# Performance work log

Hardware: AMD Instinct MI355X
Metric: run time of the kernel (lower is better)

## Reference

```python
import jax, jax.numpy as jnp
from jax import lax
import numpy as np

T, B, H, I = 128, 128, 1024, 2048  # seq, batch, hidden, lstm input (=2*H)


def lstm(x, w_ih, w_hh, b_ih, b_hh):
    """PyTorch-semantics single-layer LSTM, zero init state.
    x: [T,B,I]; w_ih: [4H,I]; w_hh: [4H,H]; gate order i,f,g,o."""
    Th, Bh = x.shape[0], x.shape[1]
    Hh = w_hh.shape[1]
    # input projection for all timesteps at once (the big GEMM)
    xp = jnp.einsum('tbi,gi->tbg', x, w_ih) + b_ih + b_hh  # [T,B,4H]

    def step(carry, xt):
        h, c = carry
        gates = xt + h @ w_hh.T  # [B,4H]
        i, f, g, o = jnp.split(gates, 4, axis=-1)
        i = jax.nn.sigmoid(i)
        f = jax.nn.sigmoid(f)
        g = jnp.tanh(g)
        o = jax.nn.sigmoid(o)
        c = f * c + i * g
        h = o * jnp.tanh(c)
        return (h, c), h

    h0 = jnp.zeros((Bh, Hh), x.dtype)
    (_, _), hs = lax.scan(step, (h0, h0), xp)
    return hs  # [T,B,H]


def setup_inputs() -> dict:
    key = jax.random.key(0)
    ks = jax.random.split(key, 10)
    s = 0.03  # ~ uniform(-1/sqrt(H), 1/sqrt(H)) scale of torch LSTM init
    return {
        'input4': jax.random.normal(ks[0], (T, B, H), jnp.float32),
        'input0': jax.random.normal(ks[1], (T, B, H), jnp.float32),
        'w_ih6': jax.random.normal(ks[2], (4 * H, I), jnp.float32) * s,
        'w_hh6': jax.random.normal(ks[3], (4 * H, H), jnp.float32) * s,
        'b_ih6': jax.random.normal(ks[4], (4 * H,), jnp.float32) * s,
        'b_hh6': jax.random.normal(ks[5], (4 * H,), jnp.float32) * s,
        'w_ih10': jax.random.normal(ks[6], (4 * H, I), jnp.float32) * s,
        'w_hh10': jax.random.normal(ks[7], (4 * H, H), jnp.float32) * s,
        'b_ih10': jax.random.normal(ks[8], (4 * H,), jnp.float32) * s,
        'b_hh10': jax.random.normal(ks[9], (4 * H,), jnp.float32) * s,
    }


def reference(input4, input0, w_ih6, w_hh6, b_ih6, b_hh6, w_ih10, w_hh10, b_ih10, b_hh10):
    out1 = input4
    out5 = jnp.concatenate([input0, out1], axis=2)        # [T,B,2H]
    out7 = lstm(out5, w_ih6, w_hh6, b_ih6, b_hh6)          # [T,B,H]
    out8 = out7  # dropout p=0.2 -> identity in eval/inference
    out9 = jnp.concatenate([out8, out1], axis=2)           # [T,B,2H]
    out11 = lstm(out9, w_ih10, w_hh10, b_ih10, b_hh10) + out7
    out13 = out11  # dropout identity
    out14 = jnp.concatenate([out13, out1], axis=2)         # [T,B,2H]
    return (out1, out11, out14)
```

## Files before the change

kernel.cpp:

```cpp
#include <hip/hip_runtime.h>
#include <hip/hip_bf16.h>
#include <hip/hip_cooperative_groups.h>
#include <stdint.h>

namespace cg = cooperative_groups;

typedef __hip_bfloat16 bf16;
typedef __attribute__((ext_vector_type(8))) short s16x8;
typedef __attribute__((ext_vector_type(4))) float f32x4;

#define MFMA_BF16 __builtin_amdgcn_mfma_f32_16x16x32_bf16


__device__ __forceinline__ float sigmoidf_(float x) {
  return 1.0f / (1.0f + __expf(-x));
}
__device__ __forceinline__ float tanhf_(float x) {
  return 2.0f / (1.0f + __expf(-2.0f * x)) - 1.0f;
}

__device__ __forceinline__ s16x8 cvt8(const float* __restrict__ p) {
  s16x8 r;
#pragma unroll
  for (int i = 0; i < 8; i++) {
    bf16 h = __float2bfloat16(p[i]);
    r[i] = *(const short*)&h;
  }
  return r;
}

__global__ __launch_bounds__(256)
void cvt_k(const float* __restrict__ src, bf16* __restrict__ dst) {
  const size_t i = (size_t)(blockIdx.x * 256 + threadIdx.x) * 8;
  *(s16x8*)(dst + i) = cvt8(src + i);
}

__global__ __launch_bounds__(256)
void gemm_xp(const void* __restrict__ A0, int a0_bf,
             const void* __restrict__ A1, int a1_bf,
             const void* __restrict__ W, int w_bf,
             const float* __restrict__ b0, const float* __restrict__ b1,
             float* __restrict__ X, int row_base)
{
  __shared__ short As[128][32];
  __shared__ short Bs[128][32];
  const int tid = threadIdx.x;
  const int wave = tid >> 6, lane = tid & 63;
  const int lr = lane & 15, lq = lane >> 4;
  const int wm = wave >> 1, wn = wave & 1;
  const int lrow0 = blockIdx.y * 128;
  const int grow0 = row_base + lrow0;
  const int col0 = blockIdx.x * 128;

  f32x4 acc[4][4];
  const f32x4 z = {0.f, 0.f, 0.f, 0.f};
  for (int i = 0; i < 4; i++)
    for (int j = 0; j < 4; j++) acc[i][j] = z;

  const int sr = tid >> 2;
  const int skk = (tid & 3) * 8;

  for (int k0 = 0; k0 < 2048; k0 += 32) {
    if (k0 < 1024) {
      if (a0_bf) {
        const bf16* Ab = (const bf16*)A0;
        *(s16x8*)&As[sr][skk]      = *(const s16x8*)(Ab + (size_t)(grow0 + sr) * 1024 + k0 + skk);
        *(s16x8*)&As[sr + 64][skk] = *(const s16x8*)(Ab + (size_t)(grow0 + sr + 64) * 1024 + k0 + skk);
      } else {
        const float* Af = (const float*)A0;
        *(s16x8*)&As[sr][skk]      = cvt8(Af + (size_t)(grow0 + sr) * 1024 + k0 + skk);
        *(s16x8*)&As[sr + 64][skk] = cvt8(Af + (size_t)(grow0 + sr + 64) * 1024 + k0 + skk);
      }
    } else {
      const int ac = k0 - 1024;
      if (a1_bf) {
        const bf16* Ab = (const bf16*)A1;
        *(s16x8*)&As[sr][skk]      = *(const s16x8*)(Ab + (size_t)(grow0 + sr) * 1024 + ac + skk);
        *(s16x8*)&As[sr + 64][skk] = *(const s16x8*)(Ab + (size_t)(grow0 + sr + 64) * 1024 + ac + skk);
      } else {
        const float* Af = (const float*)A1;
        *(s16x8*)&As[sr][skk]      = cvt8(Af + (size_t)(grow0 + sr) * 1024 + ac + skk);
        *(s16x8*)&As[sr + 64][skk] = cvt8(Af + (size_t)(grow0 + sr + 64) * 1024 + ac + skk);
      }
    }
    if (w_bf) {
      const bf16* Wb = (const bf16*)W;
      *(s16x8*)&Bs[sr][skk]      = *(const s16x8*)(Wb + (size_t)(col0 + sr) * 2048 + k0 + skk);
      *(s16x8*)&Bs[sr + 64][skk] = *(const s16x8*)(Wb + (size_t)(col0 + sr + 64) * 2048 + k0 + skk);
    } else {
      const float* Wf = (const float*)W;
      *(s16x8*)&Bs[sr][skk]      = cvt8(Wf + (size_t)(col0 + sr) * 2048 + k0 + skk);
      *(s16x8*)&Bs[sr + 64][skk] = cvt8(Wf + (size_t)(col0 + sr + 64) * 2048 + k0 + skk);
    }
    __syncthreads();
    s16x8 bfrag[4];
    for (int nt = 0; nt < 4; nt++)
      bfrag[nt] = *(const s16x8*)&Bs[wn * 64 + nt * 16 + lr][lq * 8];
    for (int mt = 0; mt < 4; mt++) {
      s16x8 a = *(const s16x8*)&As[wm * 64 + mt * 16 + lr][lq * 8];
      for (int nt = 0; nt < 4; nt++)
        acc[mt][nt] = MFMA_BF16(a, bfrag[nt], acc[mt][nt], 0, 0, 0);
    }
    __syncthreads();
  }

  for (int mt = 0; mt < 4; mt++) {
    const int mbase = lrow0 + wm * 64 + mt * 16 + lq * 4;
    for (int nt = 0; nt < 4; nt++) {
      const int n = col0 + wn * 64 + nt * 16 + lr;
      const float bias = b0[n] + b1[n];
      for (int r = 0; r < 4; r++)
        X[(size_t)(mbase + r) * 4096 + n] = acc[mt][nt][r] + bias;
    }
  }
}

__global__ __launch_bounds__(256, 1)
void lstm_chunk(const bf16* __restrict__ w_hh,
                const float* __restrict__ xp,
                float* __restrict__ c_g,
                bf16* __restrict__ hist,
                bf16* __restrict__ h2a, bf16* __restrict__ h2b,
                const bf16* __restrict__ zero,
                const bf16* __restrict__ add_base,
                float* __restrict__ o11, float* __restrict__ o14,
                int t0, int nsteps, int layer2)
{
  __shared__ __align__(16) char WS[131072];
  const int tid = threadIdx.x;
  const int wave = tid >> 6, lane = tid & 63;
  const int lr = lane & 15, lq = lane >> 4;
  const int jb = blockIdx.x & 63, mb = blockIdx.x >> 6;
  const int j0 = jb * 16;
  const int rowb = mb * 64 + wave * 16;

  for (int i = tid; i < 8192; i += 256) {
    const int rr = i >> 7, ck = i & 127;
    const int g = rr >> 4, col = rr & 15;
    const s16x8 v = *(const s16x8*)(w_hh + ((size_t)(g * 1024 + j0 + col) << 10) + (ck << 3));
    *(s16x8*)(WS + (((rr << 11) + (ck << 4)) ^ ((rr & 7) << 4))) = v;
  }

  const int j = j0 + lr;
  const int b0r = rowb + lq * 4;
  float creg[4];
#pragma unroll
  for (int r = 0; r < 4; r++) creg[r] = c_g[(b0r + r) * 1024 + j];

  const int sw = (lr & 7) << 4;
  const int rb0 = lr << 11;
  const int rb1 = (16 + lr) << 11;
  const int rb2 = (32 + lr) << 11;
  const int rb3 = (48 + lr) << 11;

  cg::grid_group grid = cg::this_grid();
  __syncthreads();

  for (int tt = 0; tt < nsteps; ++tt) {
    const int t = t0 + tt;
    const bf16* hp;
    bf16* hn;
    if (layer2) {
      hp = (t == 0) ? zero : ((t & 1) ? h2a : h2b);
      hn = (t & 1) ? h2b : h2a;
    } else {
      hp = (t == 0) ? zero : (hist + ((size_t)(t - 1) << 17));
      hn = hist + ((size_t)t << 17);
    }

    f32x4 acc[4];
    const f32x4 z = {0.f, 0.f, 0.f, 0.f};
    acc[0] = z; acc[1] = z; acc[2] = z; acc[3] = z;

    const bf16* ap = hp + ((size_t)(rowb + lr) << 10) + lq * 8;
#pragma unroll 8
    for (int k0 = 0; k0 < 1024; k0 += 32) {
      const s16x8 a = *(const s16x8*)(ap + k0);
      const int co = (((k0 >> 3) + lq) << 4) ^ sw;
      acc[0] = MFMA_BF16(a, *(const s16x8*)(WS + rb0 + co), acc[0], 0, 0, 0);
      acc[1] = MFMA_BF16(a, *(const s16x8*)(WS + rb1 + co), acc[1], 0, 0, 0);
      acc[2] = MFMA_BF16(a, *(const s16x8*)(WS + rb2 + co), acc[2], 0, 0, 0);
      acc[3] = MFMA_BF16(a, *(const s16x8*)(WS + rb3 + co), acc[3], 0, 0, 0);
    }

    const float* xpt = xp + ((size_t)tt << 19);
#pragma unroll
    for (int r = 0; r < 4; r++) {
      const int b = b0r + r;
      const float gi = acc[0][r] + xpt[b * 4096 + j];
      const float gf = acc[1][r] + xpt[b * 4096 + 1024 + j];
      const float gg = acc[2][r] + xpt[b * 4096 + 2048 + j];
      const float go = acc[3][r] + xpt[b * 4096 + 3072 + j];
      const float i_ = sigmoidf_(gi);
      const float f_ = sigmoidf_(gf);
      const float g_ = tanhf_(gg);
      const float o_ = sigmoidf_(go);
      const float cn = f_ * creg[r] + i_ * g_;
      creg[r] = cn;
      const float hv = o_ * tanhf_(cn);
      const int idx = b * 1024 + j;
      hn[idx] = __float2bfloat16(hv);
      if (layer2) {
        const float ov = hv + __bfloat162float(add_base[((size_t)t << 17) + idx]);
        o11[((size_t)t << 17) + idx] = ov;
        o14[((size_t)t << 18) + b * 2048 + j] = ov;
      }
    }

    if (tt + 1 < nsteps) grid.sync();
  }

#pragma unroll
  for (int r = 0; r < 4; r++) c_g[(b0r + r) * 1024 + j] = creg[r];
}

__global__ __launch_bounds__(256)
void finalize_k(const float4* __restrict__ in4, float4* __restrict__ out1,
                float* __restrict__ out14)
{
  const int ci = blockIdx.x * 256 + threadIdx.x;
  float4 v = in4[ci];
  out1[ci] = v;
  const int flat = ci * 4;
  const int row = flat >> 10, j = flat & 1023;
  *(float4*)&out14[(size_t)row * 2048 + 1024 + j] = v;
}

extern "C" void kernel_launch(void* const* d_in, const int* in_sizes, int n_in,
                              void* d_out, int out_size, void* d_ws, size_t ws_size,
                              hipStream_t stream)
{
  const float* input4 = (const float*)d_in[0];
  const float* input0 = (const float*)d_in[1];
  const float* w_ih6  = (const float*)d_in[2];
  const float* w_hh6  = (const float*)d_in[3];
  const float* b_ih6  = (const float*)d_in[4];
  const float* b_hh6  = (const float*)d_in[5];
  const float* w_ih10 = (const float*)d_in[6];
  const float* w_hh10 = (const float*)d_in[7];
  const float* b_ih10 = (const float*)d_in[8];
  const float* b_hh10 = (const float*)d_in[9];

  char* ws = (char*)d_ws;
  bf16* WHH6b  = (bf16*)(ws);
  bf16* WHH10b = (bf16*)(ws + 8388608ull);
  bf16* OUT7b  = (bf16*)(ws + 16777216ull);
  bf16* ZERO   = (bf16*)(ws + 50331648ull);
  bf16* H2A    = (bf16*)(ws + 50593792ull);
  bf16* H2B    = (bf16*)(ws + 50855936ull);
  float* C1    = (float*)(ws + 51118080ull);
  float* C2    = (float*)(ws + 51642368ull);

  const size_t small_bytes = 52166656ull;
  size_t avail = (ws_size > small_bytes) ? (ws_size - small_bytes) : 0;
  const size_t bf_bytes = 83886080ull;
  int TC = 16, use_bf = 0;
  if (avail >= bf_bytes + 2097152ull) {
    use_bf = 1;
    const size_t a2 = avail - bf_bytes;
    while (TC > 1 && (size_t)TC * 2097152ull > a2) TC >>= 1;
  } else {
    while (TC > 1 && (size_t)TC * 2097152ull > avail) TC >>= 1;
  }
  const int NCH = 128 / TC;
  float* Xc  = (float*)(ws + small_bytes);
  bf16* IN0b = (bf16*)(ws + small_bytes + (size_t)TC * 2097152ull);
  bf16* IN4b = IN0b + 16777216ull;
  bf16* WIHb = IN4b + 16777216ull;

  hipMemsetAsync(ZERO, 0, 262144, stream);
  hipMemsetAsync(C1, 0, 524288, stream);
  hipMemsetAsync(C2, 0, 524288, stream);

  cvt_k<<<2048, 256, 0, stream>>>(w_hh6, WHH6b);
  cvt_k<<<2048, 256, 0, stream>>>(w_hh10, WHH10b);

  float* o1  = (float*)d_out;
  float* o11 = o1 + 16777216;
  float* o14 = o1 + 33554432;

  const dim3 ggrid(32, TC);

  if (use_bf) {
    cvt_k<<<8192, 256, 0, stream>>>(input0, IN0b);
    cvt_k<<<8192, 256, 0, stream>>>(input4, IN4b);
    cvt_k<<<4096, 256, 0, stream>>>(w_ih6, WIHb);
  }
  for (int ch = 0; ch < NCH; ++ch) {
    gemm_xp<<<ggrid, 256, 0, stream>>>(
        use_bf ? (const void*)IN0b : (const void*)input0, use_bf,
        use_bf ? (const void*)IN4b : (const void*)input4, use_bf,
        use_bf ? (const void*)WIHb : (const void*)w_ih6, use_bf,
        b_ih6, b_hh6, Xc, ch * TC * 128);
    {
      const bf16* p_whh = WHH6b; const float* p_xp = Xc; float* p_c = C1;
      bf16* p_hist = OUT7b; bf16* p_h2a = nullptr; bf16* p_h2b = nullptr;
      const bf16* p_zero = ZERO; const bf16* p_add = nullptr;
      float* p_o11 = nullptr; float* p_o14 = nullptr;
      int p_t0 = ch * TC, p_ns = TC, p_l2 = 0;
      void* args[] = {&p_whh, &p_xp, &p_c, &p_hist, &p_h2a, &p_h2b,
                      &p_zero, &p_add, &p_o11, &p_o14, &p_t0, &p_ns, &p_l2};
      hipLaunchCooperativeKernel((void*)lstm_chunk, dim3(128), dim3(256),
                                 args, 0, stream);
    }
  }

  if (use_bf) {
    cvt_k<<<4096, 256, 0, stream>>>(w_ih10, WIHb);
  }
  for (int ch = 0; ch < NCH; ++ch) {
    gemm_xp<<<ggrid, 256, 0, stream>>>(
        (const void*)OUT7b, 1,
        use_bf ? (const void*)IN4b : (const void*)input4, use_bf,
        use_bf ? (const void*)WIHb : (const void*)w_ih10, use_bf,
        b_ih10, b_hh10, Xc, ch * TC * 128);
    {
      const bf16* p_whh = WHH10b; const float* p_xp = Xc; float* p_c = C2;
      bf16* p_hist = nullptr; bf16* p_h2a = H2A; bf16* p_h2b = H2B;
      const bf16* p_zero = ZERO; const bf16* p_add = OUT7b;
      float* p_o11 = o11; float* p_o14 = o14;
      int p_t0 = ch * TC, p_ns = TC, p_l2 = 1;
      void* args[] = {&p_whh, &p_xp, &p_c, &p_hist, &p_h2a, &p_h2b,
                      &p_zero, &p_add, &p_o11, &p_o14, &p_t0, &p_ns, &p_l2};
      hipLaunchCooperativeKernel((void*)lstm_chunk, dim3(128), dim3(256),
                                 args, 0, stream);
    }
  }

  finalize_k<<<16384, 256, 0, stream>>>((const float4*)input4, (float4*)d_out, o14);
}
```

Measured before the change: 7.402 ms.

## Replace cooperative grid.sync with custom atomic barrier and halve LSTM block size

Swaps cg::grid_sync for a hand-written global barrier. It uses a monotonically increasing counter with a release flag and sleep polling, and h stores are made with system-scope atomics so they are visible across blocks. Each block now runs 2 waves instead of 4, and every wave computes two 16-row M tiles, so each W_hh LDS fragment is reused twice. Layer 2 can write its h history into a separate full buffer instead of ping-pong buffers, and the time chunk grows from 16 to 32 steps, which means fewer launches. The aim is to cut barrier and launch overhead on the serial recurrence. The risks are relaxed-ordering correctness of the custom barrier and lower latency hiding with fewer waves per block.

Result: faster. 6.044 ms (-18.3%).

```diff
diff --git a/kernel.cpp b/kernel.cpp
--- a/kernel.cpp
+++ b/kernel.cpp
@@ -1,15 +1,13 @@
 #include <hip/hip_runtime.h>
 #include <hip/hip_bf16.h>
-#include <hip/hip_cooperative_groups.h>
 #include <stdint.h>
-
-namespace cg = cooperative_groups;
 
 typedef __hip_bfloat16 bf16;
 typedef __attribute__((ext_vector_type(8))) short s16x8;
 typedef __attribute__((ext_vector_type(4))) float f32x4;
 
 #define MFMA_BF16 __builtin_amdgcn_mfma_f32_16x16x32_bf16
+#define NB 128
 
 
 __device__ __forceinline__ float sigmoidf_(float x) {
@@ -115,7 +113,27 @@
   }
 }
 
-__global__ __launch_bounds__(256, 1)
+__device__ __forceinline__ void gbar_sync(unsigned* bar, unsigned target) {
+  asm volatile("s_waitcnt vmcnt(0)" ::: "memory");
+  __syncthreads();
+  if (threadIdx.x == 0) {
+    unsigned old = __hip_atomic_fetch_add(&bar[0], 1u, __ATOMIC_RELAXED,
+                                          __HIP_MEMORY_SCOPE_SYSTEM);
+    if (old == target - 1u) {
+      __hip_atomic_store(&bar[64], target, __ATOMIC_RELAXED,
+                         __HIP_MEMORY_SCOPE_SYSTEM);
+    } else {
+      while (__hip_atomic_load(&bar[64], __ATOMIC_RELAXED,
+                               __HIP_MEMORY_SCOPE_SYSTEM) < target) {
+        __builtin_amdgcn_s_sleep(1);
+      }
+    }
+    __builtin_amdgcn_fence(__ATOMIC_ACQUIRE, "agent");
+  }
+  __syncthreads();
+}
+
+__global__ __launch_bounds__(128, 1)
 void lstm_chunk(const bf16* __restrict__ w_hh,
                 const float* __restrict__ xp,
                 float* __restrict__ c_g,
@@ -124,6 +142,7 @@
                 const bf16* __restrict__ zero,
                 const bf16* __restrict__ add_base,
                 float* __restrict__ o11, float* __restrict__ o14,
+                unsigned* __restrict__ bar, unsigned gbase,
                 int t0, int nsteps, int layer2)
 {
   __shared__ __align__(16) char WS[131072];
@@ -132,9 +151,9 @@
   const int lr = lane & 15, lq = lane >> 4;
   const int jb = blockIdx.x & 63, mb = blockIdx.x >> 6;
   const int j0 = jb * 16;
-  const int rowb = mb * 64 + wave * 16;
-
-  for (int i = tid; i < 8192; i += 256) {
+  const int wrow = mb * 64 + wave * 32;
+
+  for (int i = tid; i < 8192; i += 128) {
     const int rr = i >> 7, ck = i & 127;
     const int g = rr >> 4, col = rr & 15;
     const s16x8 v = *(const s16x8*)(w_hh + ((size_t)(g * 1024 + j0 + col) << 10) + (ck << 3));
@@ -142,76 +161,96 @@
   }
 
   const int j = j0 + lr;
-  const int b0r = rowb + lq * 4;
-  float creg[4];
-#pragma unroll
-  for (int r = 0; r < 4; r++) creg[r] = c_g[(b0r + r) * 1024 + j];
-
   const int sw = (lr & 7) << 4;
-  const int rb0 = lr << 11;
-  const int rb1 = (16 + lr) << 11;
-  const int rb2 = (32 + lr) << 11;
-  const int rb3 = (48 + lr) << 11;
-
-  cg::grid_group grid = cg::this_grid();
+  int rbg[4];
+#pragma unroll
+  for (int g = 0; g < 4; g++) rbg[g] = (g * 16 + lr) << 11;
+
+  float creg[2][4];
+#pragma unroll
+  for (int mt = 0; mt < 2; mt++)
+#pragma unroll
+    for (int r = 0; r < 4; r++)
+      creg[mt][r] = c_g[(wrow + mt * 16 + lq * 4 + r) * 1024 + j];
+
   __syncthreads();
 
   for (int tt = 0; tt < nsteps; ++tt) {
     const int t = t0 + tt;
     const bf16* hp;
     bf16* hn;
-    if (layer2) {
+    if (hist) {
+      hp = (t == 0) ? zero : (hist + ((size_t)(t - 1) << 17));
+      hn = hist + ((size_t)t << 17);
+    } else {
       hp = (t == 0) ? zero : ((t & 1) ? h2a : h2b);
       hn = (t & 1) ? h2b : h2a;
-    } else {
-      hp = (t == 0) ? zero : (hist + ((size_t)(t - 1) << 17));
-      hn = hist + ((size_t)t << 17);
-    }
-
-    f32x4 acc[4];
+    }
+
+    f32x4 acc[2][4];
     const f32x4 z = {0.f, 0.f, 0.f, 0.f};
-    acc[0] = z; acc[1] = z; acc[2] = z; acc[3] = z;
-
-    const bf16* ap = hp + ((size_t)(rowb + lr) << 10) + lq * 8;
+#pragma unroll
+    for (int mt = 0; mt < 2; mt++)
+#pragma unroll
+      for (int g = 0; g < 4; g++) acc[mt][g] = z;
+
+    const bf16* ap0 = hp + ((size_t)(wrow + lr) << 10) + lq * 8;
 #pragma unroll 8
     for (int k0 = 0; k0 < 1024; k0 += 32) {
-      const s16x8 a = *(const s16x8*)(ap + k0);
+      const s16x8 a0 = *(const s16x8*)(ap0 + k0);
+      const s16x8 a1 = *(const s16x8*)(ap0 + 16384 + k0);
       const int co = (((k0 >> 3) + lq) << 4) ^ sw;
-      acc[0] = MFMA_BF16(a, *(const s16x8*)(WS + rb0 + co), acc[0], 0, 0, 0);
-      acc[1] = MFMA_BF16(a, *(const s16x8*)(WS + rb1 + co), acc[1], 0, 0, 0);
-      acc[2] = MFMA_BF16(a, *(const s16x8*)(WS + rb2 + co), acc[2], 0, 0, 0);
-      acc[3] = MFMA_BF16(a, *(const s16x8*)(WS + rb3 + co), acc[3], 0, 0, 0);
+      s16x8 b[4];
+#pragma unroll
+      for (int g = 0; g < 4; g++)
+        b[g] = *(const s16x8*)(WS + rbg[g] + co);
+#pragma unroll
+      for (int g = 0; g < 4; g++)
+        acc[0][g] = MFMA_BF16(a0, b[g], acc[0][g], 0, 0, 0);
+#pragma unroll
+      for (int g = 0; g < 4; g++)
+        acc[1][g] = MFMA_BF16(a1, b[g], acc[1][g], 0, 0, 0);
     }
 
     const float* xpt = xp + ((size_t)tt << 19);
 #pragma unroll
-    for (int r = 0; r < 4; r++) {
-      const int b = b0r + r;
-      const float gi = acc[0][r] + xpt[b * 4096 + j];
-      const float gf = acc[1][r] + xpt[b * 4096 + 1024 + j];
-      const float gg = acc[2][r] + xpt[b * 4096 + 2048 + j];
-      const float go = acc[3][r] + xpt[b * 4096 + 3072 + j];
-      const float i_ = sigmoidf_(gi);
-      const float f_ = sigmoidf_(gf);
-      const float g_ = tanhf_(gg);
-      const float o_ = sigmoidf_(go);
-      const float cn = f_ * creg[r] + i_ * g_;
-      creg[r] = cn;
-      const float hv = o_ * tanhf_(cn);
-      const int idx = b * 1024 + j;
-      hn[idx] = __float2bfloat16(hv);
-      if (layer2) {
-        const float ov = hv + __bfloat162float(add_base[((size_t)t << 17) + idx]);
-        o11[((size_t)t << 17) + idx] = ov;
-        o14[((size_t)t << 18) + b * 2048 + j] = ov;
+    for (int mt = 0; mt < 2; mt++) {
+#pragma unroll
+      for (int r = 0; r < 4; r++) {
+        const int b = wrow + mt * 16 + lq * 4 + r;
+        const float gi = acc[mt][0][r] + xpt[b * 4096 + j];
+        const float gf = acc[mt][1][r] + xpt[b * 4096 + 1024 + j];
+        const float gg = acc[mt][2][r] + xpt[b * 4096 + 2048 + j];
+        const float go = acc[mt][3][r] + xpt[b * 4096 + 3072 + j];
+        const float i_ = sigmoidf_(gi);
+        const float f_ = sigmoidf_(gf);
+        const float g_ = tanhf_(gg);
+        const float o_ = sigmoidf_(go);
+        const float cn = f_ * creg[mt][r] + i_ * g_;
+        creg[mt][r] = cn;
+        const float hv = o_ * tanhf_(cn);
+        const int idx = b * 1024 + j;
+        bf16 hb = __float2bfloat16(hv);
+        __hip_atomic_store((unsigned short*)(hn + idx),
+                           *(unsigned short*)&hb,
+                           __ATOMIC_RELAXED, __HIP_MEMORY_SCOPE_SYSTEM);
+        if (layer2) {
+          const float ov = hv + __bfloat162float(add_base[((size_t)t << 17) + idx]);
+          o11[((size_t)t << 17) + idx] = ov;
+          o14[((size_t)t << 18) + b * 2048 + j] = ov;
+        }
       }
     }
 
-    if (tt + 1 < nsteps) grid.sync();
-  }
-
-#pragma unroll
-  for (int r = 0; r < 4; r++) c_g[(b0r + r) * 1024 + j] = creg[r];
+    if (tt + 1 < nsteps)
+      gbar_sync(bar, gbase + (unsigned)(tt + 1) * NB);
+  }
+
+#pragma unroll
+  for (int mt = 0; mt < 2; mt++)
+#pragma unroll
+    for (int r = 0; r < 4; r++)
+      c_g[(wrow + mt * 16 + lq * 4 + r) * 1024 + j] = creg[mt][r];
 }
 
 __global__ __launch_bounds__(256)
@@ -250,11 +289,21 @@
   bf16* H2B    = (bf16*)(ws + 50855936ull);
   float* C1    = (float*)(ws + 51118080ull);
   float* C2    = (float*)(ws + 51642368ull);
-
-  const size_t small_bytes = 52166656ull;
-  size_t avail = (ws_size > small_bytes) ? (ws_size - small_bytes) : 0;
+  unsigned* BAR = (unsigned*)(ws + 52166656ull);
+
+  const size_t base_end = 52170752ull;
+  size_t avail = (ws_size > base_end) ? (ws_size - base_end) : 0;
+  size_t off = base_end;
+  int use_h2h = 0;
+  bf16* H2H = nullptr;
+  if (avail >= 33554432ull + 2097152ull) {
+    use_h2h = 1;
+    H2H = (bf16*)(ws + off);
+    off += 33554432ull;
+    avail -= 33554432ull;
+  }
   const size_t bf_bytes = 83886080ull;
-  int TC = 16, use_bf = 0;
+  int TC = 32, use_bf = 0;
   if (avail >= bf_bytes + 2097152ull) {
     use_bf = 1;
     const size_t a2 = avail - bf_bytes;
@@ -263,14 +312,15 @@
     while (TC > 1 && (size_t)TC * 2097152ull > avail) TC >>= 1;
   }
   const int NCH = 128 / TC;
-  float* Xc  = (float*)(ws + small_bytes);
-  bf16* IN0b = (bf16*)(ws + small_bytes + (size_t)TC * 2097152ull);
+  float* Xc  = (float*)(ws + off);
+  bf16* IN0b = (bf16*)(ws + off + (size_t)TC * 2097152ull);
   bf16* IN4b = IN0b + 16777216ull;
   bf16* WIHb = IN4b + 16777216ull;
 
   hipMemsetAsync(ZERO, 0, 262144, stream);
   hipMemsetAsync(C1, 0, 524288, stream);
   hipMemsetAsync(C2, 0, 524288, stream);
+  hipMemsetAsync(BAR, 0, 4096, stream);
 
   cvt_k<<<2048, 256, 0, stream>>>(w_hh6, WHH6b);
   cvt_k<<<2048, 256, 0, stream>>>(w_hh10, WHH10b);
@@ -280,6 +330,7 @@
   float* o14 = o1 + 33554432;
 
   const dim3 ggrid(32, TC);
+  unsigned gbase = 0;
 
   if (use_bf) {
     cvt_k<<<8192, 256, 0, stream>>>(input0, IN0b);
@@ -297,11 +348,14 @@
       bf16* p_hist = OUT7b; bf16* p_h2a = nullptr; bf16* p_h2b = nullptr;
       const bf16* p_zero = ZERO; const bf16* p_add = nullptr;
       float* p_o11 = nullptr; float* p_o14 = nullptr;
+      unsigned* p_bar = BAR; unsigned p_gb = gbase;
       int p_t0 = ch * TC, p_ns = TC, p_l2 = 0;
       void* args[] = {&p_whh, &p_xp, &p_c, &p_hist, &p_h2a, &p_h2b,
-                      &p_zero, &p_add, &p_o11, &p_o14, &p_t0, &p_ns, &p_l2};
-      hipLaunchCooperativeKernel((void*)lstm_chunk, dim3(128), dim3(256),
+                      &p_zero, &p_add, &p_o11, &p_o14, &p_bar, &p_gb,
+                      &p_t0, &p_ns, &p_l2};
+      hipLaunchCooperativeKernel((void*)lstm_chunk, dim3(NB), dim3(128),
                                  args, 0, stream);
+      gbase += (unsigned)NB * (unsigned)(TC - 1);
     }
   }
 
@@ -316,14 +370,18 @@
         b_ih10, b_hh10, Xc, ch * TC * 128);
     {
       const bf16* p_whh = WHH10b; const float* p_xp = Xc; float* p_c = C2;
-      bf16* p_hist = nullptr; bf16* p_h2a = H2A; bf16* p_h2b = H2B;
+      bf16* p_hist = use_h2h ? H2H : nullptr;
+      bf16* p_h2a = H2A; bf16* p_h2b = H2B;
       const bf16* p_zero = ZERO; const bf16* p_add = OUT7b;
       float* p_o11 = o11; float* p_o14 = o14;
+      unsigned* p_bar = BAR; unsigned p_gb = gbase;
       int p_t0 = ch * TC, p_ns = TC, p_l2 = 1;
       void* args[] = {&p_whh, &p_xp, &p_c, &p_hist, &p_h2a, &p_h2b,
-                      &p_zero, &p_add, &p_o11, &p_o14, &p_t0, &p_ns, &p_l2};
-      hipLaunchCooperativeKernel((void*)lstm_chunk, dim3(128), dim3(256),
+                      &p_zero, &p_add, &p_o11, &p_o14, &p_bar, &p_gb,
+                      &p_t0, &p_ns, &p_l2};
+      hipLaunchCooperativeKernel((void*)lstm_chunk, dim3(NB), dim3(128),
                                  args, 0, stream);
+      gbase += (unsigned)NB * (unsigned)(TC - 1);
     }
   }
 
```
